# Kernel tuning notes

Measured on AMD Instinct MI355X. Metric: run time of the kernel, lower is better.

The kernel has to match this reference:

```python
import jax, jax.numpy as jnp
import numpy as np

B = 64
N = 8192
C = 91
MAX_PRED = 300
NUM_SEL = 8000


def setup_inputs() -> dict:
    key = jax.random.key(0)
    k1, k2, k3, k4, k5 = jax.random.split(key, 5)
    pred_boxes = jax.random.normal(k1, (B, N, 4), dtype=jnp.float32)
    pred_scores = jax.random.uniform(k2, (B, N, C), dtype=jnp.float32)
    batch_idx = jax.random.randint(k3, (NUM_SEL,), 0, B, dtype=jnp.int64)
    label_idx = jax.random.randint(k4, (NUM_SEL,), 0, C, dtype=jnp.int64)
    box_idx = jax.random.randint(k5, (NUM_SEL,), 0, N, dtype=jnp.int64)
    selected_indexes = jnp.stack([batch_idx, label_idx, box_idx], axis=1)
    return {"pred_boxes": pred_boxes, "pred_scores": pred_scores, "selected_indexes": selected_indexes}


def reference(pred_boxes, pred_scores, selected_indexes):
    # selected_indexes rows: [batch_index, label_index, box_index]
    b = selected_indexes[:, 0]
    lab = selected_indexes[:, 1]
    box = selected_indexes[:, 2]

    sel_boxes = pred_boxes[b, box]          # [S, 4]
    sel_scores = pred_scores[b, box, lab]   # [S]

    # Per-batch stable rank of each selected row (position inside its image).
    onehot = (b[:, None] == jnp.arange(B, dtype=b.dtype)[None, :]).astype(jnp.int32)  # [S, B]
    rank = jnp.take_along_axis(jnp.cumsum(onehot, axis=0), b[:, None].astype(jnp.int32), axis=1)[:, 0] - 1  # [S]

    rows = jnp.concatenate(
        [sel_boxes, sel_scores[:, None], lab[:, None].astype(pred_boxes.dtype)], axis=1
    )  # [S, 6] = [x1,y1,x2,y2,score,class]

    # Scatter-compact into padded per-image slots; out-of-range ranks dropped
    # (original torch code assumes <= MAX_PRED per image and would error otherwise).
    rank_c = jnp.where(rank < MAX_PRED, rank, MAX_PRED)
    batched = jnp.zeros((B, MAX_PRED, 6), dtype=pred_boxes.dtype).at[b, rank_c].set(rows, mode="drop")

    num_predictions = jax.ops.segment_sum(jnp.ones_like(b, dtype=jnp.int32), b, num_segments=B)  # [B]

    out_boxes = batched[:, :, 0:4]
    out_scores = batched[:, :, 4]
    out_classes = batched[:, :, 5].astype(jnp.int32)
    return num_predictions[:, None], out_boxes, out_scores, out_classes
```

## Files before the change

### kernel.cpp

```cpp
#include <hip/hip_runtime.h>

#define BATCH 64
#define NBOX 8192
#define NCLS 91
#define MAX_PRED 300
#define NUM_SEL 8000
#define NWORDS 125

__global__ __launch_bounds__(256)
void pick_nms_kernel(const float* __restrict__ pred_boxes,
                     const float* __restrict__ pred_scores,
                     const int* __restrict__ sel,
                     float* __restrict__ out) {
    const int b    = blockIdx.x;
    const int tid  = threadIdx.x;
    const int lane = tid & 63;
    const int wid  = tid >> 6;

    __shared__ unsigned long long masks[NWORDS];
    __shared__ int excl[NWORDS];
    __shared__ int wave_tot[4];
    __shared__ int perm[MAX_PRED];

    float* out_num     = out;
    float* out_boxes   = out + BATCH;
    float* out_scores  = out + BATCH + BATCH*MAX_PRED*4;
    float* out_classes = out + BATCH + BATCH*MAX_PRED*5;

    int bv[32];
    #pragma unroll
    for (int k = 0; k < 32; ++k) {
        const int i = k * 256 + tid;
        bv[k] = (i < NUM_SEL) ? sel[3 * i] : -1;
    }
    #pragma unroll
    for (int k = 0; k < 32; ++k) {
        const unsigned long long m = __ballot(bv[k] == b);
        const int w = k * 4 + wid;
        if (lane == 0 && w < NWORDS) masks[w] = m;
    }
    __syncthreads();

    const int mypc = (tid < NWORDS) ? __popcll(masks[tid]) : 0;
    int incl = mypc;
    #pragma unroll
    for (int d = 1; d < 64; d <<= 1) {
        const int n = __shfl_up(incl, d, 64);
        if (lane >= d) incl += n;
    }
    if (lane == 63) wave_tot[wid] = incl;
    __syncthreads();
    const int woff = (wid == 1) ? wave_tot[0] : 0;
    if (tid < NWORDS) excl[tid] = woff + incl - mypc;
    const int cnt = wave_tot[0] + wave_tot[1];
    __syncthreads();

    const unsigned long long lane_mask = (1ull << lane) - 1ull;
    #pragma unroll
    for (int k = 0; k < 32; ++k) {
        const unsigned long long m = __ballot(bv[k] == b);
        if (bv[k] == b) {
            const int w = k * 4 + wid;
            const int rank = excl[w] + __popcll(m & lane_mask);
            if (rank < MAX_PRED) perm[rank] = k * 256 + tid;
        }
    }
    __syncthreads();

    const int lim = (cnt < MAX_PRED) ? cnt : MAX_PRED;
    #pragma unroll
    for (int rr = 0; rr < 2; ++rr) {
        const int r = tid + rr * 256;
        if (r < MAX_PRED) {
            float4 bx = make_float4(0.f, 0.f, 0.f, 0.f);
            float sc = 0.f, cls = 0.f;
            if (r < lim) {
                const int i   = perm[r];
                const int lab = sel[3 * i + 1];
                const int box = sel[3 * i + 2];
                bx  = *reinterpret_cast<const float4*>(pred_boxes + ((size_t)b*NBOX + box)*4);
                sc  = pred_scores[((size_t)b*NBOX + box)*NCLS + lab];
                cls = (float)lab;
            }
            *reinterpret_cast<float4*>(out_boxes + ((size_t)b*MAX_PRED + r)*4) = bx;
            out_scores[b*MAX_PRED + r]  = sc;
            out_classes[b*MAX_PRED + r] = cls;
        }
    }
    if (tid == 0) out_num[b] = (float)cnt;
}

extern "C" void kernel_launch(void* const* d_in, const int* in_sizes, int n_in,
                              void* d_out, int out_size, void* d_ws, size_t ws_size,
                              hipStream_t stream) {
    const float* pred_boxes  = (const float*)d_in[0];
    const float* pred_scores = (const float*)d_in[1];
    const int*   sel         = (const int*)d_in[2];
    float* out = (float*)d_out;

    pick_nms_kernel<<<dim3(BATCH), dim3(256), 0, stream>>>(
        pred_boxes, pred_scores, sel, out);
}
```

Measured before the change: 11.04 us.

## Load full selection triples once, stash label/box in LDS, widen block to 512

Each thread now reads whole (batch, label, box) triples during the initial scan and keeps label and box in registers. The compacted rows are written to shared memory as label/box pairs, so the final gather no longer re-reads the selection array through a permutation index. The block grows to 512 threads, which halves the per-thread loop count, and the prefix scan over mask words is reduced to a single wave that handles two words per lane, removing one barrier. The cost is more registers per thread and every block loading all triples instead of only the batch column.

```diff
diff --git a/kernel.cpp b/kernel.cpp
--- a/kernel.cpp
+++ b/kernel.cpp
@@ -6,86 +6,97 @@
 #define MAX_PRED 300
 #define NUM_SEL 8000
 #define NWORDS 125
+#define NT 512
+#define KCH 16
 
-__global__ __launch_bounds__(256)
+struct __align__(4) Int3 { int x, y, z; };
+
+__global__ __launch_bounds__(NT)
 void pick_nms_kernel(const float* __restrict__ pred_boxes,
                      const float* __restrict__ pred_scores,
-                     const int* __restrict__ sel,
+                     const Int3* __restrict__ sel,
                      float* __restrict__ out) {
     const int b    = blockIdx.x;
     const int tid  = threadIdx.x;
     const int lane = tid & 63;
     const int wid  = tid >> 6;
 
-    __shared__ unsigned long long masks[NWORDS];
-    __shared__ int excl[NWORDS];
-    __shared__ int wave_tot[4];
-    __shared__ int perm[MAX_PRED];
+    __shared__ unsigned long long masks[NWORDS + 1];
+    __shared__ int  excl[NWORDS + 1];
+    __shared__ int2 lb[MAX_PRED];
+    __shared__ int  cnt_s;
 
     float* out_num     = out;
     float* out_boxes   = out + BATCH;
     float* out_scores  = out + BATCH + BATCH*MAX_PRED*4;
     float* out_classes = out + BATCH + BATCH*MAX_PRED*5;
 
-    int bv[32];
+    if (tid < 2) masks[NWORDS + tid - 1] = 0ull;
+
+    int bv[KCH], lab[KCH], box[KCH];
     #pragma unroll
-    for (int k = 0; k < 32; ++k) {
-        const int i = k * 256 + tid;
-        bv[k] = (i < NUM_SEL) ? sel[3 * i] : -1;
+    for (int k = 0; k < KCH; ++k) {
+        const int i = k * NT + tid;
+        if (i < NUM_SEL) {
+            const Int3 v = sel[i];
+            bv[k] = v.x; lab[k] = v.y; box[k] = v.z;
+        } else {
+            bv[k] = -1; lab[k] = 0; box[k] = 0;
+        }
     }
     #pragma unroll
-    for (int k = 0; k < 32; ++k) {
+    for (int k = 0; k < KCH; ++k) {
         const unsigned long long m = __ballot(bv[k] == b);
-        const int w = k * 4 + wid;
+        const int w = k * 8 + wid;
         if (lane == 0 && w < NWORDS) masks[w] = m;
     }
     __syncthreads();
 
-    const int mypc = (tid < NWORDS) ? __popcll(masks[tid]) : 0;
-    int incl = mypc;
-    #pragma unroll
-    for (int d = 1; d < 64; d <<= 1) {
-        const int n = __shfl_up(incl, d, 64);
-        if (lane >= d) incl += n;
+    if (wid == 0) {
+        const int t = lane;
+        const int p0 = (2*t     < NWORDS) ? __popcll(masks[2*t])     : 0;
+        const int p1 = (2*t + 1 < NWORDS) ? __popcll(masks[2*t + 1]) : 0;
+        int incl = p0 + p1;
+        #pragma unroll
+        for (int d = 1; d < 64; d <<= 1) {
+            const int n = __shfl_up(incl, d, 64);
+            if (t >= d) incl += n;
+        }
+        const int e0 = incl - p1 - p0;
+        if (2*t < NWORDS)     excl[2*t]     = e0;
+        if (2*t + 1 < NWORDS) excl[2*t + 1] = e0 + p0;
+        const int total = __shfl(incl, 62, 64);
+        if (t == 0) cnt_s = total;
     }
-    if (lane == 63) wave_tot[wid] = incl;
     __syncthreads();
-    const int woff = (wid == 1) ? wave_tot[0] : 0;
-    if (tid < NWORDS) excl[tid] = woff + incl - mypc;
-    const int cnt = wave_tot[0] + wave_tot[1];
-    __syncthreads();
+    const int cnt = cnt_s;
 
     const unsigned long long lane_mask = (1ull << lane) - 1ull;
     #pragma unroll
-    for (int k = 0; k < 32; ++k) {
+    for (int k = 0; k < KCH; ++k) {
         const unsigned long long m = __ballot(bv[k] == b);
         if (bv[k] == b) {
-            const int w = k * 4 + wid;
+            const int w = k * 8 + wid;
             const int rank = excl[w] + __popcll(m & lane_mask);
-            if (rank < MAX_PRED) perm[rank] = k * 256 + tid;
+            if (rank < MAX_PRED) lb[rank] = make_int2(lab[k], box[k]);
         }
     }
     __syncthreads();
 
     const int lim = (cnt < MAX_PRED) ? cnt : MAX_PRED;
-    #pragma unroll
-    for (int rr = 0; rr < 2; ++rr) {
-        const int r = tid + rr * 256;
-        if (r < MAX_PRED) {
-            float4 bx = make_float4(0.f, 0.f, 0.f, 0.f);
-            float sc = 0.f, cls = 0.f;
-            if (r < lim) {
-                const int i   = perm[r];
-                const int lab = sel[3 * i + 1];
-                const int box = sel[3 * i + 2];
-                bx  = *reinterpret_cast<const float4*>(pred_boxes + ((size_t)b*NBOX + box)*4);
-                sc  = pred_scores[((size_t)b*NBOX + box)*NCLS + lab];
-                cls = (float)lab;
-            }
-            *reinterpret_cast<float4*>(out_boxes + ((size_t)b*MAX_PRED + r)*4) = bx;
-            out_scores[b*MAX_PRED + r]  = sc;
-            out_classes[b*MAX_PRED + r] = cls;
+    if (tid < MAX_PRED) {
+        const int r = tid;
+        float4 bx = make_float4(0.f, 0.f, 0.f, 0.f);
+        float sc = 0.f, cls = 0.f;
+        if (r < lim) {
+            const int2 v = lb[r];
+            bx  = *reinterpret_cast<const float4*>(pred_boxes + ((size_t)b*NBOX + v.y)*4);
+            sc  = pred_scores[((size_t)b*NBOX + v.y)*NCLS + v.x];
+            cls = (float)v.x;
         }
+        *reinterpret_cast<float4*>(out_boxes + ((size_t)b*MAX_PRED + r)*4) = bx;
+        out_scores[b*MAX_PRED + r]  = sc;
+        out_classes[b*MAX_PRED + r] = cls;
     }
     if (tid == 0) out_num[b] = (float)cnt;
 }
@@ -95,9 +106,9 @@
                               hipStream_t stream) {
     const float* pred_boxes  = (const float*)d_in[0];
     const float* pred_scores = (const float*)d_in[1];
-    const int*   sel         = (const int*)d_in[2];
+    const Int3*  sel         = (const Int3*)d_in[2];
     float* out = (float*)d_out;
 
-    pick_nms_kernel<<<dim3(BATCH), dim3(256), 0, stream>>>(
+    pick_nms_kernel<<<dim3(BATCH), dim3(NT), 0, stream>>>(
         pred_boxes, pred_scores, sel, out);
 }
```

Result: faster. 9.770 us (-11.5%).
